# Kernel optimization log

Measured on AMD Instinct MI355X. Metric: run time of the kernel, lower is better.

## Reference

```python
import jax, jax.numpy as jnp
import numpy as np

EMBED_DIM = 64
CODEBOOK_SIZE = 1024


def setup_inputs() -> dict:
    key = jax.random.key(0)
    k1, k2 = jax.random.split(key)
    inputs = jax.random.normal(k1, (32, 4096, EMBED_DIM), dtype=jnp.float32)
    # codebook stored as (embedding_dim, codebook_size), as in the TF layer
    embeddings = jax.random.normal(k2, (EMBED_DIM, CODEBOOK_SIZE), dtype=jnp.float32)
    return {"inputs": inputs, "embeddings": embeddings}


def reference(inputs, embeddings):
    # inputs: [B, T, D]; embeddings: [D, K]
    B, T, D = inputs.shape
    K = embeddings.shape[1]
    flat = inputs.reshape(-1, D)  # [N, D]
    similarity = flat @ embeddings  # [N, K]
    distances = (
        jnp.sum(flat * flat, axis=1, keepdims=True)
        - 2.0 * similarity
        + jnp.sum(embeddings * embeddings, axis=0, keepdims=True)
    )
    # temperature==0 / inference path -> plain argmax(-distances) == argmin(distances)
    encoding_indices_flat = jnp.argmin(distances, axis=1)  # [N]
    encodings = jax.nn.one_hot(encoding_indices_flat, K, dtype=jnp.float32)  # [N, K]
    encoding_indices = encoding_indices_flat.reshape(B, T)
    # embedding lookup on transposed codebook: [K, D] gathered -> [B, T, D]
    quantized = embeddings.T[encoding_indices]
    # straight-through estimator
    quantized_st = inputs + jax.lax.stop_gradient(quantized - inputs)
    return quantized_st, encodings, encoding_indices
```

## Files before the change

kernel.cpp:

```cpp
#include <hip/hip_runtime.h>

#define D 64
#define K 1024
#define NTOK (32 * 4096)
#define Q_ELEMS ((size_t)NTOK * D)
#define OH_ELEMS ((size_t)NTOK * K)

typedef short bf16x8 __attribute__((ext_vector_type(8)));
typedef float f32x4 __attribute__((ext_vector_type(4)));

#define WS_ETF_OFF 4096
#define WS_ETH_OFF (4096 + 262144)
#define WS_ETL_OFF (4096 + 262144 + 131072)
#define WS_NEED    (4096 + 262144 + 131072 + 131072)

__device__ __forceinline__ unsigned short f2bf(float f) {
    unsigned u = __float_as_uint(f);
    unsigned r = u + 0x7FFFu + ((u >> 16) & 1u);
    return (unsigned short)(r >> 16);
}
__device__ __forceinline__ float bf2f(unsigned short h) {
    return __uint_as_float(((unsigned)h) << 16);
}

__global__ void prep_kernel(const float* __restrict__ E, float* __restrict__ ws) {
    int k = blockIdx.x * 256 + threadIdx.x;
    float* e2 = ws;
    float* etf = (float*)((char*)ws + WS_ETF_OFF);
    unsigned short* ethF = (unsigned short*)((char*)ws + WS_ETH_OFF);
    unsigned short* etlF = (unsigned short*)((char*)ws + WS_ETL_OFF);

    const int tile = k >> 6, ct = (k >> 4) & 3, l15 = k & 15;
    float s = 0.f;
    #pragma unroll
    for (int d = 0; d < D; ++d) {
        float v = E[d * K + k];
        s = fmaf(v, v, s);
        etf[k * D + d] = v;
        unsigned short h = f2bf(v);
        unsigned short l = f2bf(v - bf2f(h));
        const int ks = d >> 5, g = (d >> 3) & 3, j = d & 7;
        const int slot = (((tile * 4 + ct) * 2 + ks) * 64 + g * 16 + l15) * 8 + j;
        ethF[slot] = h;
        etlF[slot] = l;
    }
    e2[k] = s;
}

__device__ __attribute__((noinline)) int rescore_token(
    const float* __restrict__ X, const float* __restrict__ E,
    const float* __restrict__ e2g, int tok, int lane)
{
    const float* xr = X + (size_t)tok * D;
    float bestv = 3.4e38f; int besti = 0;
    #pragma unroll 1
    for (int sb = 0; sb < 2; ++sb) {
        const int k0 = lane * 16 + sb * 8;
        float dot[8] = {0.f,0.f,0.f,0.f,0.f,0.f,0.f,0.f};
        #pragma unroll 1
        for (int db = 0; db < 4; ++db) {
            float4 xc0 = *reinterpret_cast<const float4*>(xr + db * 16 + 0);
            float4 xc1 = *reinterpret_cast<const float4*>(xr + db * 16 + 4);
            float4 xc2 = *reinterpret_cast<const float4*>(xr + db * 16 + 8);
            float4 xc3 = *reinterpret_cast<const float4*>(xr + db * 16 + 12);
            float xs[16] = {xc0.x,xc0.y,xc0.z,xc0.w, xc1.x,xc1.y,xc1.z,xc1.w,
                            xc2.x,xc2.y,xc2.z,xc2.w, xc3.x,xc3.y,xc3.z,xc3.w};
            #pragma unroll
            for (int dd = 0; dd < 16; ++dd) {
                const int d = db * 16 + dd;
                float4 e0 = *reinterpret_cast<const float4*>(E + (size_t)d * K + k0);
                float4 e1 = *reinterpret_cast<const float4*>(E + (size_t)d * K + k0 + 4);
                dot[0] = fmaf(xs[dd], e0.x, dot[0]); dot[1] = fmaf(xs[dd], e0.y, dot[1]);
                dot[2] = fmaf(xs[dd], e0.z, dot[2]); dot[3] = fmaf(xs[dd], e0.w, dot[3]);
                dot[4] = fmaf(xs[dd], e1.x, dot[4]); dot[5] = fmaf(xs[dd], e1.y, dot[5]);
                dot[6] = fmaf(xs[dd], e1.z, dot[6]); dot[7] = fmaf(xs[dd], e1.w, dot[7]);
            }
        }
        float4 ez0 = *reinterpret_cast<const float4*>(e2g + k0);
        float4 ez1 = *reinterpret_cast<const float4*>(e2g + k0 + 4);
        float ezs[8] = {ez0.x,ez0.y,ez0.z,ez0.w, ez1.x,ez1.y,ez1.z,ez1.w};
        #pragma unroll
        for (int j = 0; j < 8; ++j) {
            float dist = fmaf(-2.f, dot[j], ezs[j]);
            if (dist < bestv) { bestv = dist; besti = k0 + j; }
        }
    }
    #pragma unroll
    for (int mm = 1; mm <= 32; mm <<= 1) {
        float ob = __shfl_xor(bestv, mm, 64);
        int   oi = __shfl_xor(besti, mm, 64);
        bool take = (ob < bestv) || (ob == bestv && oi < besti);
        bestv = take ? ob : bestv;
        besti = take ? oi : besti;
    }
    return besti;
}

__global__ __launch_bounds__(256, 3) void vq_mfma_kernel(
    const float* __restrict__ X,
    const float* __restrict__ E,
    const float* __restrict__ ws_f,
    float* __restrict__ qout,
    float* __restrict__ oneh,
    float* __restrict__ idxout)
{
    __shared__ __align__(16) unsigned short btile[2][2][8][512];

    const int lane   = threadIdx.x & 63;
    const int wv     = threadIdx.x >> 6;
    const int lane15 = lane & 15;
    const int g      = lane >> 4;
    const int tokbase = blockIdx.x * 128 + wv * 32;

    const float* e2g = ws_f;
    const float* etf = (const float*)((const char*)ws_f + WS_ETF_OFF);
    const char* ethB = (const char*)ws_f + WS_ETH_OFF;
    const char* etlB = (const char*)ws_f + WS_ETL_OFF;

    bf16x8 ah[2][2], al[2][2];
    #pragma unroll
    for (int mt = 0; mt < 2; ++mt) {
        const float* xr = X + (size_t)(tokbase + mt * 16 + lane15) * D + g * 8;
        #pragma unroll
        for (int ks = 0; ks < 2; ++ks) {
            float4 v0 = *reinterpret_cast<const float4*>(xr + ks * 32);
            float4 v1 = *reinterpret_cast<const float4*>(xr + ks * 32 + 4);
            float xv[8] = {v0.x,v0.y,v0.z,v0.w, v1.x,v1.y,v1.z,v1.w};
            #pragma unroll
            for (int j = 0; j < 8; ++j) {
                unsigned short h = f2bf(xv[j]);
                ah[mt][ks][j] = (short)h;
                al[mt][ks][j] = (short)f2bf(xv[j] - bf2f(h));
            }
        }
    }

    float bb[2][4] = {{3.4e38f,3.4e38f,3.4e38f,3.4e38f},{3.4e38f,3.4e38f,3.4e38f,3.4e38f}};
    float b2[2][4] = {{3.4e38f,3.4e38f,3.4e38f,3.4e38f},{3.4e38f,3.4e38f,3.4e38f,3.4e38f}};
    int   bi[2][4] = {{0,0,0,0},{0,0,0,0}};

    #define GLOAD_TILE(T, B)                                                          \
        do {                                                                          \
            _Pragma("unroll")                                                         \
            for (int cc = 0; cc < 4; ++cc) {                                          \
                const int c = wv * 4 + cc;                                            \
                const char* src = ((c < 8) ? ethB : etlB)                             \
                                  + (size_t)(T) * 8192 + (size_t)(c & 7) * 1024       \
                                  + (size_t)lane * 16;                                \
                __builtin_amdgcn_global_load_lds(                                     \
                    (const __attribute__((address_space(1))) void*)src,               \
                    (__attribute__((address_space(3))) void*)&btile[B][c >> 3][c & 7][0], \
                    16, 0, 0);                                                        \
            }                                                                         \
        } while (0)

    GLOAD_TILE(0, 0);

    #pragma unroll 1
    for (int tile = 0; tile < 16; ++tile) {
        const int buf = tile & 1;
        __syncthreads();
        if (tile < 15) GLOAD_TILE(tile + 1, buf ^ 1);

        #pragma unroll
        for (int ct = 0; ct < 4; ++ct) {
            const int code = tile * 64 + ct * 16 + lane15;
            f32x4 acc0 = {0.f,0.f,0.f,0.f};
            f32x4 acc1 = {0.f,0.f,0.f,0.f};
            #pragma unroll
            for (int ks = 0; ks < 2; ++ks) {
                const int slot = ct * 2 + ks;
                bf16x8 bh = reinterpret_cast<const bf16x8*>(&btile[buf][0][slot][0])[lane];
                bf16x8 bl = reinterpret_cast<const bf16x8*>(&btile[buf][1][slot][0])[lane];
                acc0 = __builtin_amdgcn_mfma_f32_16x16x32_bf16(ah[0][ks], bh, acc0, 0, 0, 0);
                acc0 = __builtin_amdgcn_mfma_f32_16x16x32_bf16(ah[0][ks], bl, acc0, 0, 0, 0);
                acc0 = __builtin_amdgcn_mfma_f32_16x16x32_bf16(al[0][ks], bh, acc0, 0, 0, 0);
                acc1 = __builtin_amdgcn_mfma_f32_16x16x32_bf16(ah[1][ks], bh, acc1, 0, 0, 0);
                acc1 = __builtin_amdgcn_mfma_f32_16x16x32_bf16(ah[1][ks], bl, acc1, 0, 0, 0);
                acc1 = __builtin_amdgcn_mfma_f32_16x16x32_bf16(al[1][ks], bh, acc1, 0, 0, 0);
            }
            const float e2v = e2g[code];
            #pragma unroll
            for (int r = 0; r < 4; ++r) {
                float d0 = fmaf(-2.f, acc0[r], e2v);
                b2[0][r] = fminf(b2[0][r], fmaxf(bb[0][r], d0));
                if (d0 < bb[0][r]) { bb[0][r] = d0; bi[0][r] = code; }
                float d1 = fmaf(-2.f, acc1[r], e2v);
                b2[1][r] = fminf(b2[1][r], fmaxf(bb[1][r], d1));
                if (d1 < bb[1][r]) { bb[1][r] = d1; bi[1][r] = code; }
            }
        }
    }

    #pragma unroll
    for (int m = 1; m <= 8; m <<= 1) {
        #pragma unroll
        for (int mt = 0; mt < 2; ++mt) {
            #pragma unroll
            for (int r = 0; r < 4; ++r) {
                float ob = __shfl_xor(bb[mt][r], m, 64);
                float o2 = __shfl_xor(b2[mt][r], m, 64);
                int   oi = __shfl_xor(bi[mt][r], m, 64);
                float nb2 = fminf(fminf(b2[mt][r], o2), fmaxf(bb[mt][r], ob));
                bool take = (ob < bb[mt][r]) || (ob == bb[mt][r] && oi < bi[mt][r]);
                bb[mt][r] = take ? ob : bb[mt][r];
                bi[mt][r] = take ? oi : bi[mt][r];
                b2[mt][r] = nb2;
            }
        }
    }

    #pragma unroll
    for (int mt = 0; mt < 2; ++mt) {
        #pragma unroll
        for (int r = 0; r < 4; ++r) {
            bool flag = (b2[mt][r] - bb[mt][r]) < 0.125f;
            unsigned long long m = __ballot(flag);
            if (m) {
                #pragma unroll
                for (int gg = 0; gg < 4; ++gg) {
                    if ((m >> (gg * 16)) & 1ULL) {
                        int ei = rescore_token(X, E, e2g, tokbase + mt * 16 + gg * 4 + r, lane);
                        if (g == gg) bi[mt][r] = ei;
                    }
                }
            }
        }
    }

    #pragma unroll
    for (int t = 0; t < 32; ++t) {
        const int t16 = t & 15;
        const int fi = __shfl(bi[t >> 4][t16 & 3], (t16 >> 2) * 16, 64);
        const size_t tok = (size_t)tokbase + t;

        float q  = etf[(size_t)fi * D + lane];
        float xv = X[tok * D + lane];
        __builtin_nontemporal_store(xv + (q - xv), qout + tok * D + lane);

        if (lane == t) idxout[tok] = (float)fi;

        f32x4* row = reinterpret_cast<f32x4*>(oneh + tok * (size_t)K);
        #pragma unroll
        for (int c = 0; c < 4; ++c) {
            const int c4 = (c * 64 + lane) * 4;
            f32x4 v;
            v[0] = (fi == c4 + 0) ? 1.f : 0.f;
            v[1] = (fi == c4 + 1) ? 1.f : 0.f;
            v[2] = (fi == c4 + 2) ? 1.f : 0.f;
            v[3] = (fi == c4 + 3) ? 1.f : 0.f;
            __builtin_nontemporal_store(v, row + c * 64 + lane);
        }
    }
}

__global__ __launch_bounds__(256, 2) void vq_fallback_kernel(
    const float* __restrict__ X, const float* __restrict__ E,
    float* __restrict__ qout, float* __restrict__ oneh, float* __restrict__ idxout)
{
    __shared__ float e2s[K];
    __shared__ int   idxs[256];
    const int tid = threadIdx.x;
    const int tok = blockIdx.x * 256 + tid;
    for (int k = tid; k < K; k += 256) {
        float s = 0.f;
        #pragma unroll
        for (int d = 0; d < D; ++d) { float v = E[d * K + k]; s = fmaf(v, v, s); }
        e2s[k] = s;
    }
    __syncthreads();
    float x[D];
    {
        const float* xp = X + (size_t)tok * D;
        #pragma unroll
        for (int j = 0; j < D / 4; ++j) {
            float4 v = *reinterpret_cast<const float4*>(xp + 4 * j);
            x[4*j+0]=v.x; x[4*j+1]=v.y; x[4*j+2]=v.z; x[4*j+3]=v.w;
        }
    }
    float best = 3.4e38f; int bidx = 0;
    for (int t0 = 0; t0 < K; t0 += 16) {
        float acc[16];
        #pragma unroll
        for (int j = 0; j < 16; ++j) acc[j] = 0.f;
        #pragma unroll
        for (int d = 0; d < D; ++d) {
            const float* ep = E + d * K + t0;
            #pragma unroll
            for (int j = 0; j < 16; ++j) acc[j] = fmaf(x[d], ep[j], acc[j]);
        }
        #pragma unroll
        for (int j = 0; j < 16; ++j) {
            float dist = fmaf(-2.f, acc[j], e2s[t0 + j]);
            if (dist < best) { best = dist; bidx = t0 + j; }
        }
    }
    idxs[tid] = bidx;
    {
        float q[D];
        const float* ec = E + bidx;
        #pragma unroll
        for (int d = 0; d < D; ++d) q[d] = ec[d * K];
        float* qp = qout + (size_t)tok * D;
        #pragma unroll
        for (int j = 0; j < D / 4; ++j) {
            float4 v;
            v.x = x[4*j+0] + (q[4*j+0] - x[4*j+0]);
            v.y = x[4*j+1] + (q[4*j+1] - x[4*j+1]);
            v.z = x[4*j+2] + (q[4*j+2] - x[4*j+2]);
            v.w = x[4*j+3] + (q[4*j+3] - x[4*j+3]);
            *reinterpret_cast<float4*>(qp + 4 * j) = v;
        }
    }
    idxout[tok] = (float)bidx;
    __syncthreads();
    {
        float4* base = reinterpret_cast<float4*>(oneh + (size_t)blockIdx.x * 256 * K);
        for (int i = tid; i < 256 * K / 4; i += 256) {
            int row = i >> 8, c4 = (i & 255) * 4, id = idxs[row];
            float4 v;
            v.x = (id == c4 + 0) ? 1.f : 0.f;
            v.y = (id == c4 + 1) ? 1.f : 0.f;
            v.z = (id == c4 + 2) ? 1.f : 0.f;
            v.w = (id == c4 + 3) ? 1.f : 0.f;
            base[i] = v;
        }
    }
}

extern "C" void kernel_launch(void* const* d_in, const int* in_sizes, int n_in,
                              void* d_out, int out_size, void* d_ws, size_t ws_size,
                              hipStream_t stream) {
    const float* X = (const float*)d_in[0];
    const float* E = (const float*)d_in[1];
    float* qout   = (float*)d_out;
    float* oneh   = qout + Q_ELEMS;
    float* idxout = oneh + OH_ELEMS;

    if (ws_size >= (size_t)WS_NEED) {
        float* ws = (float*)d_ws;
        prep_kernel<<<K / 256, 256, 0, stream>>>(E, ws);
        vq_mfma_kernel<<<NTOK / 128, 256, 0, stream>>>(X, E, ws, qout, oneh, idxout);
    } else {
        vq_fallback_kernel<<<NTOK / 256, 256, 0, stream>>>(X, E, qout, oneh, idxout);
    }
}
```

Baseline: 216.3 us.

## Warp-specialize VQ kernel: producer waves zero one-hot while compute waves run MFMA

The block grows to 512 threads. Four waves run the MFMA distance and argmin search as before. The other four waves write zeros to the block's one-hot rows during the tile loop, staying in step through the shared __syncthreads calls. Afterwards the indices are passed through shared memory, and the writer waves scatter the single 1.0 per row and write the quantized output and indices. The aim is to overlap the large one-hot store traffic with the compute phase, at the cost of more threads per block, lower occupancy per CU, and a second write to each one-hot row.

```diff
diff --git a/kernel.cpp b/kernel.cpp
--- a/kernel.cpp
+++ b/kernel.cpp
@@ -96,7 +96,7 @@
     return besti;
 }
 
-__global__ __launch_bounds__(256, 3) void vq_mfma_kernel(
+__global__ __launch_bounds__(512, 4) void vq_fused_kernel(
     const float* __restrict__ X,
     const float* __restrict__ E,
     const float* __restrict__ ws_f,
@@ -105,151 +105,171 @@
     float* __restrict__ idxout)
 {
     __shared__ __align__(16) unsigned short btile[2][2][8][512];
-
-    const int lane   = threadIdx.x & 63;
-    const int wv     = threadIdx.x >> 6;
-    const int lane15 = lane & 15;
-    const int g      = lane >> 4;
-    const int tokbase = blockIdx.x * 128 + wv * 32;
+    __shared__ int idxs[128];
+
+    const int lane = threadIdx.x & 63;
+    const int wave = threadIdx.x >> 6;
+    const size_t blkTok = (size_t)blockIdx.x * 128;
 
     const float* e2g = ws_f;
     const float* etf = (const float*)((const char*)ws_f + WS_ETF_OFF);
     const char* ethB = (const char*)ws_f + WS_ETH_OFF;
     const char* etlB = (const char*)ws_f + WS_ETL_OFF;
 
-    bf16x8 ah[2][2], al[2][2];
-    #pragma unroll
-    for (int mt = 0; mt < 2; ++mt) {
-        const float* xr = X + (size_t)(tokbase + mt * 16 + lane15) * D + g * 8;
-        #pragma unroll
-        for (int ks = 0; ks < 2; ++ks) {
-            float4 v0 = *reinterpret_cast<const float4*>(xr + ks * 32);
-            float4 v1 = *reinterpret_cast<const float4*>(xr + ks * 32 + 4);
-            float xv[8] = {v0.x,v0.y,v0.z,v0.w, v1.x,v1.y,v1.z,v1.w};
-            #pragma unroll
-            for (int j = 0; j < 8; ++j) {
-                unsigned short h = f2bf(xv[j]);
-                ah[mt][ks][j] = (short)h;
-                al[mt][ks][j] = (short)f2bf(xv[j] - bf2f(h));
-            }
-        }
-    }
-
-    float bb[2][4] = {{3.4e38f,3.4e38f,3.4e38f,3.4e38f},{3.4e38f,3.4e38f,3.4e38f,3.4e38f}};
-    float b2[2][4] = {{3.4e38f,3.4e38f,3.4e38f,3.4e38f},{3.4e38f,3.4e38f,3.4e38f,3.4e38f}};
-    int   bi[2][4] = {{0,0,0,0},{0,0,0,0}};
-
-    #define GLOAD_TILE(T, B)                                                          \
-        do {                                                                          \
-            _Pragma("unroll")                                                         \
-            for (int cc = 0; cc < 4; ++cc) {                                          \
-                const int c = wv * 4 + cc;                                            \
-                const char* src = ((c < 8) ? ethB : etlB)                             \
-                                  + (size_t)(T) * 8192 + (size_t)(c & 7) * 1024       \
-                                  + (size_t)lane * 16;                                \
-                __builtin_amdgcn_global_load_lds(                                     \
-                    (const __attribute__((address_space(1))) void*)src,               \
-                    (__attribute__((address_space(3))) void*)&btile[B][c >> 3][c & 7][0], \
-                    16, 0, 0);                                                        \
-            }                                                                         \
-        } while (0)
-
-    GLOAD_TILE(0, 0);
-
-    #pragma unroll 1
-    for (int tile = 0; tile < 16; ++tile) {
-        const int buf = tile & 1;
+    if (wave < 4) {
+        const int wv     = wave;
+        const int lane15 = lane & 15;
+        const int g      = lane >> 4;
+        const int tokbase = (int)blkTok + wv * 32;
+
+        bf16x8 ah[2][2], al[2][2];
+        #pragma unroll
+        for (int mt = 0; mt < 2; ++mt) {
+            const float* xr = X + (size_t)(tokbase + mt * 16 + lane15) * D + g * 8;
+            #pragma unroll
+            for (int ks = 0; ks < 2; ++ks) {
+                float4 v0 = *reinterpret_cast<const float4*>(xr + ks * 32);
+                float4 v1 = *reinterpret_cast<const float4*>(xr + ks * 32 + 4);
+                float xv[8] = {v0.x,v0.y,v0.z,v0.w, v1.x,v1.y,v1.z,v1.w};
+                #pragma unroll
+                for (int j = 0; j < 8; ++j) {
+                    unsigned short h = f2bf(xv[j]);
+                    ah[mt][ks][j] = (short)h;
+                    al[mt][ks][j] = (short)f2bf(xv[j] - bf2f(h));
+                }
+            }
+        }
+
+        float bb[2][4] = {{3.4e38f,3.4e38f,3.4e38f,3.4e38f},{3.4e38f,3.4e38f,3.4e38f,3.4e38f}};
+        float b2[2][4] = {{3.4e38f,3.4e38f,3.4e38f,3.4e38f},{3.4e38f,3.4e38f,3.4e38f,3.4e38f}};
+        int   bi[2][4] = {{0,0,0,0},{0,0,0,0}};
+
+        #define GLOAD_TILE(T, B)                                                      \
+            do {                                                                      \
+                _Pragma("unroll")                                                     \
+                for (int cc = 0; cc < 4; ++cc) {                                      \
+                    const int c = wv * 4 + cc;                                        \
+                    const char* src = ((c < 8) ? ethB : etlB)                         \
+                                      + (size_t)(T) * 8192 + (size_t)(c & 7) * 1024   \
+                                      + (size_t)lane * 16;                            \
+                    __builtin_amdgcn_global_load_lds(                                 \
+                        (const __attribute__((address_space(1))) void*)src,           \
+                        (__attribute__((address_space(3))) void*)&btile[B][c >> 3][c & 7][0], \
+                        16, 0, 0);                                                    \
+                }                                                                     \
+            } while (0)
+
+        GLOAD_TILE(0, 0);
+
+        #pragma unroll 1
+        for (int tile = 0; tile < 16; ++tile) {
+            const int buf = tile & 1;
+            __syncthreads();
+            if (tile < 15) GLOAD_TILE(tile + 1, buf ^ 1);
+
+            #pragma unroll
+            for (int ct = 0; ct < 4; ++ct) {
+                const int code = tile * 64 + ct * 16 + lane15;
+                f32x4 acc0 = {0.f,0.f,0.f,0.f};
+                f32x4 acc1 = {0.f,0.f,0.f,0.f};
+                #pragma unroll
+                for (int ks = 0; ks < 2; ++ks) {
+                    const int slot = ct * 2 + ks;
+                    bf16x8 bh = reinterpret_cast<const bf16x8*>(&btile[buf][0][slot][0])[lane];
+                    bf16x8 bl = reinterpret_cast<const bf16x8*>(&btile[buf][1][slot][0])[lane];
+                    acc0 = __builtin_amdgcn_mfma_f32_16x16x32_bf16(ah[0][ks], bh, acc0, 0, 0, 0);
+                    acc0 = __builtin_amdgcn_mfma_f32_16x16x32_bf16(ah[0][ks], bl, acc0, 0, 0, 0);
+                    acc0 = __builtin_amdgcn_mfma_f32_16x16x32_bf16(al[0][ks], bh, acc0, 0, 0, 0);
+                    acc1 = __builtin_amdgcn_mfma_f32_16x16x32_bf16(ah[1][ks], bh, acc1, 0, 0, 0);
+                    acc1 = __builtin_amdgcn_mfma_f32_16x16x32_bf16(ah[1][ks], bl, acc1, 0, 0, 0);
+                    acc1 = __builtin_amdgcn_mfma_f32_16x16x32_bf16(al[1][ks], bh, acc1, 0, 0, 0);
+                }
+                const float e2v = e2g[code];
+                #pragma unroll
+                for (int r = 0; r < 4; ++r) {
+                    float d0 = fmaf(-2.f, acc0[r], e2v);
+                    b2[0][r] = fminf(b2[0][r], fmaxf(bb[0][r], d0));
+                    if (d0 < bb[0][r]) { bb[0][r] = d0; bi[0][r] = code; }
+                    float d1 = fmaf(-2.f, acc1[r], e2v);
+                    b2[1][r] = fminf(b2[1][r], fmaxf(bb[1][r], d1));
+                    if (d1 < bb[1][r]) { bb[1][r] = d1; bi[1][r] = code; }
+                }
+            }
+        }
+
+        #pragma unroll
+        for (int m = 1; m <= 8; m <<= 1) {
+            #pragma unroll
+            for (int mt = 0; mt < 2; ++mt) {
+                #pragma unroll
+                for (int r = 0; r < 4; ++r) {
+                    float ob = __shfl_xor(bb[mt][r], m, 64);
+                    float o2 = __shfl_xor(b2[mt][r], m, 64);
+                    int   oi = __shfl_xor(bi[mt][r], m, 64);
+                    float nb2 = fminf(fminf(b2[mt][r], o2), fmaxf(bb[mt][r], ob));
+                    bool take = (ob < bb[mt][r]) || (ob == bb[mt][r] && oi < bi[mt][r]);
+                    bb[mt][r] = take ? ob : bb[mt][r];
+                    bi[mt][r] = take ? oi : bi[mt][r];
+                    b2[mt][r] = nb2;
+                }
+            }
+        }
+
+        #pragma unroll
+        for (int mt = 0; mt < 2; ++mt) {
+            #pragma unroll
+            for (int r = 0; r < 4; ++r) {
+                bool flag = (b2[mt][r] - bb[mt][r]) < 0.125f;
+                unsigned long long m = __ballot(flag);
+                if (m) {
+                    #pragma unroll
+                    for (int gg = 0; gg < 4; ++gg) {
+                        if ((m >> (gg * 16)) & 1ULL) {
+                            int ei = rescore_token(X, E, e2g, tokbase + mt * 16 + gg * 4 + r, lane);
+                            if (g == gg) bi[mt][r] = ei;
+                        }
+                    }
+                }
+            }
+        }
+
+        if (lane15 == 0) {
+            #pragma unroll
+            for (int mt = 0; mt < 2; ++mt)
+                #pragma unroll
+                for (int r = 0; r < 4; ++r)
+                    idxs[wv * 32 + mt * 16 + g * 4 + r] = bi[mt][r];
+        }
         __syncthreads();
-        if (tile < 15) GLOAD_TILE(tile + 1, buf ^ 1);
-
-        #pragma unroll
-        for (int ct = 0; ct < 4; ++ct) {
-            const int code = tile * 64 + ct * 16 + lane15;
-            f32x4 acc0 = {0.f,0.f,0.f,0.f};
-            f32x4 acc1 = {0.f,0.f,0.f,0.f};
-            #pragma unroll
-            for (int ks = 0; ks < 2; ++ks) {
-                const int slot = ct * 2 + ks;
-                bf16x8 bh = reinterpret_cast<const bf16x8*>(&btile[buf][0][slot][0])[lane];
-                bf16x8 bl = reinterpret_cast<const bf16x8*>(&btile[buf][1][slot][0])[lane];
-                acc0 = __builtin_amdgcn_mfma_f32_16x16x32_bf16(ah[0][ks], bh, acc0, 0, 0, 0);
-                acc0 = __builtin_amdgcn_mfma_f32_16x16x32_bf16(ah[0][ks], bl, acc0, 0, 0, 0);
-                acc0 = __builtin_amdgcn_mfma_f32_16x16x32_bf16(al[0][ks], bh, acc0, 0, 0, 0);
-                acc1 = __builtin_amdgcn_mfma_f32_16x16x32_bf16(ah[1][ks], bh, acc1, 0, 0, 0);
-                acc1 = __builtin_amdgcn_mfma_f32_16x16x32_bf16(ah[1][ks], bl, acc1, 0, 0, 0);
-                acc1 = __builtin_amdgcn_mfma_f32_16x16x32_bf16(al[1][ks], bh, acc1, 0, 0, 0);
-            }
-            const float e2v = e2g[code];
-            #pragma unroll
-            for (int r = 0; r < 4; ++r) {
-                float d0 = fmaf(-2.f, acc0[r], e2v);
-                b2[0][r] = fminf(b2[0][r], fmaxf(bb[0][r], d0));
-                if (d0 < bb[0][r]) { bb[0][r] = d0; bi[0][r] = code; }
-                float d1 = fmaf(-2.f, acc1[r], e2v);
-                b2[1][r] = fminf(b2[1][r], fmaxf(bb[1][r], d1));
-                if (d1 < bb[1][r]) { bb[1][r] = d1; bi[1][r] = code; }
-            }
-        }
-    }
-
-    #pragma unroll
-    for (int m = 1; m <= 8; m <<= 1) {
-        #pragma unroll
-        for (int mt = 0; mt < 2; ++mt) {
-            #pragma unroll
-            for (int r = 0; r < 4; ++r) {
-                float ob = __shfl_xor(bb[mt][r], m, 64);
-                float o2 = __shfl_xor(b2[mt][r], m, 64);
-                int   oi = __shfl_xor(bi[mt][r], m, 64);
-                float nb2 = fminf(fminf(b2[mt][r], o2), fmaxf(bb[mt][r], ob));
-                bool take = (ob < bb[mt][r]) || (ob == bb[mt][r] && oi < bi[mt][r]);
-                bb[mt][r] = take ? ob : bb[mt][r];
-                bi[mt][r] = take ? oi : bi[mt][r];
-                b2[mt][r] = nb2;
-            }
-        }
-    }
-
-    #pragma unroll
-    for (int mt = 0; mt < 2; ++mt) {
-        #pragma unroll
-        for (int r = 0; r < 4; ++r) {
-            bool flag = (b2[mt][r] - bb[mt][r]) < 0.125f;
-            unsigned long long m = __ballot(flag);
-            if (m) {
-                #pragma unroll
-                for (int gg = 0; gg < 4; ++gg) {
-                    if ((m >> (gg * 16)) & 1ULL) {
-                        int ei = rescore_token(X, E, e2g, tokbase + mt * 16 + gg * 4 + r, lane);
-                        if (g == gg) bi[mt][r] = ei;
-                    }
-                }
-            }
-        }
-    }
-
-    #pragma unroll
-    for (int t = 0; t < 32; ++t) {
-        const int t16 = t & 15;
-        const int fi = __shfl(bi[t >> 4][t16 & 3], (t16 >> 2) * 16, 64);
-        const size_t tok = (size_t)tokbase + t;
-
-        float q  = etf[(size_t)fi * D + lane];
-        float xv = X[tok * D + lane];
-        __builtin_nontemporal_store(xv + (q - xv), qout + tok * D + lane);
-
-        if (lane == t) idxout[tok] = (float)fi;
-
-        f32x4* row = reinterpret_cast<f32x4*>(oneh + tok * (size_t)K);
-        #pragma unroll
-        for (int c = 0; c < 4; ++c) {
-            const int c4 = (c * 64 + lane) * 4;
-            f32x4 v;
-            v[0] = (fi == c4 + 0) ? 1.f : 0.f;
-            v[1] = (fi == c4 + 1) ? 1.f : 0.f;
-            v[2] = (fi == c4 + 2) ? 1.f : 0.f;
-            v[3] = (fi == c4 + 3) ? 1.f : 0.f;
-            __builtin_nontemporal_store(v, row + c * 64 + lane);
+    } else {
+        const int w = wave - 4;
+        f32x4* ohz = reinterpret_cast<f32x4*>(oneh + (blkTok + (size_t)w * 32) * K);
+        const f32x4 zv = {0.f, 0.f, 0.f, 0.f};
+
+        #pragma unroll 1
+        for (int t = 0; t < 16; ++t) {
+            __syncthreads();
+            #pragma unroll
+            for (int zi = 0; zi < 8; ++zi)
+                __builtin_nontemporal_store(zv, ohz + (t * 8 + zi) * 64 + lane);
+        }
+        __syncthreads();
+
+        const int tokbase = (int)blkTok + w * 32;
+
+        if (lane < 32) {
+            int fi = idxs[w * 32 + lane];
+            oneh[(size_t)(tokbase + lane) * K + fi] = 1.0f;
+            idxout[tokbase + lane] = (float)fi;
+        }
+
+        #pragma unroll 1
+        for (int t = 0; t < 32; ++t) {
+            int fi = idxs[w * 32 + t];
+            const size_t tok = (size_t)tokbase + t;
+            float q  = etf[(size_t)fi * D + lane];
+            float xv = X[tok * D + lane];
+            __builtin_nontemporal_store(xv + (q - xv), qout + tok * D + lane);
         }
     }
 }
@@ -340,7 +360,7 @@
     if (ws_size >= (size_t)WS_NEED) {
         float* ws = (float*)d_ws;
         prep_kernel<<<K / 256, 256, 0, stream>>>(E, ws);
-        vq_mfma_kernel<<<NTOK / 128, 256, 0, stream>>>(X, E, ws, qout, oneh, idxout);
+        vq_fused_kernel<<<NTOK / 128, 512, 0, stream>>>(X, E, ws, qout, oneh, idxout);
     } else {
         vq_fallback_kernel<<<NTOK / 256, 256, 0, stream>>>(X, E, qout, oneh, idxout);
     }
```

New measurement: 252.0 us. 1.16x slower.
